# Kernel optimization log

Hardware: AMD Instinct MI355X
Metric: run time of the kernel (lower is better)

Reference implementation:

```python
import jax, jax.numpy as jnp
import numpy as np

S, B, E, H = 512, 64, 256, 256


def _cell(h, c, xt, wih, whh, bih, bhh):
    # PyTorch LSTM gate order: i, f, g, o
    z = xt @ wih.T + h @ whh.T + bih + bhh  # (B, 4H)
    i, f, g, o = jnp.split(z, 4, axis=-1)
    c = jax.nn.sigmoid(f) * c + jax.nn.sigmoid(i) * jnp.tanh(g)
    h = jax.nn.sigmoid(o) * jnp.tanh(c)
    return h, c


def _bilstm(x, h0, c0, wih_f, whh_f, bih_f, bhh_f, wih_b, whh_b, bih_b, bhh_b):
    # x: (T,B,E); h0,c0: (2,B,H) -> out (T,B,2H), hn/cn (2,B,H)
    def fstep(carry, xt):
        h, c = _cell(carry[0], carry[1], xt, wih_f, whh_f, bih_f, bhh_f)
        return (h, c), h

    def bstep(carry, xt):
        h, c = _cell(carry[0], carry[1], xt, wih_b, whh_b, bih_b, bhh_b)
        return (h, c), h

    (hf, cf), out_f = jax.lax.scan(fstep, (h0[0], c0[0]), x)
    (hb, cb), out_b_rev = jax.lax.scan(bstep, (h0[1], c0[1]), x[::-1])
    out = jnp.concatenate([out_f, out_b_rev[::-1]], axis=-1)
    return out, jnp.stack([hf, hb]), jnp.stack([cf, cb])


def setup_inputs() -> dict:
    key = jax.random.key(0)
    ks = jax.random.split(key, 9)
    s = 1.0 / np.sqrt(H)
    u = lambda k, shape: jax.random.uniform(k, shape, jnp.float32, -s, s)
    return {
        "inputs": jax.random.normal(ks[0], (S, B, E), jnp.float32),
        "wih_f": u(ks[1], (4 * H, E)), "whh_f": u(ks[2], (4 * H, H)),
        "bih_f": u(ks[3], (4 * H,)), "bhh_f": u(ks[4], (4 * H,)),
        "wih_b": u(ks[5], (4 * H, E)), "whh_b": u(ks[6], (4 * H, H)),
        "bih_b": u(ks[7], (4 * H,)), "bhh_b": u(ks[8], (4 * H,)),
    }


def reference(inputs, wih_f, whh_f, bih_f, bhh_f, wih_b, whh_b, bih_b, bhh_b):
    seq, batch = inputs.shape[0], inputs.shape[1]
    params = (wih_f, whh_f, bih_f, bhh_f, wih_b, whh_b, bih_b, bhh_b)
    # windows i=0..S-2 are each 2 tokens: inputs[i:i+2]
    windows = jnp.stack([inputs[:-1], inputs[1:]], axis=1)  # (S-1, 2, B, E)

    def step(carry, win):
        h, c = carry
        out, hn, cn = _bilstm(win, h, c, *params)
        return (hn, cn), out  # out (2,B,2H)

    h0 = jnp.zeros((2, batch, H), inputs.dtype)
    c0 = jnp.zeros((2, batch, H), inputs.dtype)
    (hl, cl), outs = jax.lax.scan(step, (h0, c0), windows)
    # final window i=S-1 is length 1, seeded with the state from window S-2
    out_last, _, _ = _bilstm(inputs[-1:], hl, cl, *params)  # (1,B,2H)
    hidden = jnp.concatenate(
        [outs.reshape(2 * (seq - 1), batch, 2 * H), out_last], axis=0
    )  # (2S-1, B, 2H)
    # AdaptiveMaxPool1d(1) over the time axis
    emb = hidden.max(axis=0)  # (B, 2H)
    return emb
```

## Files before the change

kernel.cpp:

```cpp
#include <hip/hip_runtime.h>

typedef __attribute__((ext_vector_type(8))) short short8;
typedef __attribute__((ext_vector_type(4))) float f32x4;
typedef __attribute__((ext_vector_type(4))) unsigned short u16x4;
typedef __attribute__((ext_vector_type(4))) unsigned int u32x4;

#define S_ 512
#define B_ 64
#define E_ 256
#define H_ 256
#define NSTEP 1023

__device__ __forceinline__ unsigned short f2bf(float f) {
  unsigned u = __builtin_bit_cast(unsigned, f);
  return (unsigned short)((u + 0x7fffu + ((u >> 16) & 1u)) >> 16);
}
__device__ __forceinline__ float bf2f(unsigned short h) {
  unsigned u = ((unsigned)h) << 16;
  return __builtin_bit_cast(float, u);
}
__device__ __forceinline__ float sigm(float x) { return 1.f / (1.f + __expf(-x)); }
__device__ __forceinline__ float tanh_(float x) {
  x = fminf(fmaxf(x, -15.f), 15.f);
  float e = __expf(-2.f * x);
  return (1.f - e) / (1.f + e);
}

__global__ __launch_bounds__(256) void prep9(
    const float* __restrict__ x,
    const float* __restrict__ wih_f, const float* __restrict__ whh_f,
    const float* __restrict__ bih_f, const float* __restrict__ bhh_f,
    const float* __restrict__ wih_b, const float* __restrict__ whh_b,
    const float* __restrict__ bih_b, const float* __restrict__ bhh_b,
    short* __restrict__ x_bf, short* __restrict__ wx, short* __restrict__ wh,
    float* __restrict__ bias_p)
{
  long i0 = (long)blockIdx.x * blockDim.x + threadIdx.x;
  long stride = (long)gridDim.x * blockDim.x;
  const long NX = (long)S_ * B_ * E_;
  const long NW = 2L * 1024 * 256;
  const long NB = 2L * 1024;

  for (long i = i0; i < NX; i += stride) x_bf[i] = (short)f2bf(x[i]);

  for (long i = i0; i < NW; i += stride) {
    int ch  = (int)(i >> 18);
    int rem = (int)(i & 262143);
    int p   = rem >> 8;
    int k   = rem & 255;
    int jc  = p >> 2, g = p & 3;
    long j  = (long)(g * 256 + jc);
    wx[i] = (short)f2bf((ch ? wih_b : wih_f)[j * 256 + k]);
    wh[i] = (short)f2bf((ch ? whh_b : whh_f)[j * 256 + k]);
  }

  for (long i = i0; i < NB; i += stride) {
    int ch = (int)(i >> 10);
    int p  = (int)(i & 1023);
    int jc = p >> 2, g = p & 3;
    int j  = g * 256 + jc;
    bias_p[i] = ch ? (bih_b[j] + bhh_b[j]) : (bih_f[j] + bhh_f[j]);
  }
}

__global__ __launch_bounds__(512, 2) void xz_gemm9(
    const short* __restrict__ x_bf, const short* __restrict__ wx,
    const float* __restrict__ bias_p, short* __restrict__ xz)
{
  const int bid = blockIdx.x;
  const int ch = bid >> 9, t = bid & 511;
  const int tid = threadIdx.x;
  const int wave = tid >> 6, lane = tid & 63;
  const int l15 = lane & 15, l4 = lane >> 4;

  const short* W = wx + (long)ch * 1024 * 256;
  const short* X = x_bf + (long)t * B_ * E_;

  f32x4 acc[8][4];
#pragma unroll
  for (int mt = 0; mt < 8; ++mt)
#pragma unroll
    for (int nt = 0; nt < 4; ++nt) acc[mt][nt] = (f32x4){0.f, 0.f, 0.f, 0.f};

#pragma unroll
  for (int ks = 0; ks < 8; ++ks) {
    int k0 = ks * 32 + l4 * 8;
    short8 bfr[4];
#pragma unroll
    for (int nt = 0; nt < 4; ++nt)
      bfr[nt] = *(const short8*)(X + (long)(nt * 16 + l15) * E_ + k0);
#pragma unroll
    for (int mt = 0; mt < 8; ++mt) {
      int p = (wave * 8 + mt) * 16 + l15;
      short8 af = *(const short8*)(W + (long)p * 256 + k0);
#pragma unroll
      for (int nt = 0; nt < 4; ++nt)
        acc[mt][nt] = __builtin_amdgcn_mfma_f32_16x16x32_bf16(af, bfr[nt], acc[mt][nt], 0, 0, 0);
    }
  }

#pragma unroll
  for (int mt = 0; mt < 8; ++mt) {
    int jc = (wave * 8 + mt) * 4 + l4;
    f32x4 b4 = *(const f32x4*)(bias_p + ch * 1024 + jc * 4);
#pragma unroll
    for (int nt = 0; nt < 4; ++nt) {
      int b = nt * 16 + l15;
      u16x4 v;
#pragma unroll
      for (int g = 0; g < 4; ++g) v[g] = f2bf(acc[mt][nt][g] + b4[g]);
      long off = (((long)(ch * 512 + t) * 256 + jc) * 64 + b) * 4;
      *(u16x4*)(xz + off) = v;
    }
  }
}

__global__ __launch_bounds__(512) void lstm10(
    const short* __restrict__ wh, const short* __restrict__ xz,
    short* __restrict__ hring, float* __restrict__ out)
{
  const int bid  = blockIdx.x;
  const int ch   = bid >> 4;
  const int bs   = (bid >> 2) & 3;
  const int role = bid & 3;
  const int tid  = threadIdx.x;
  const int wave = tid >> 6, lane = tid & 63;
  const int l15 = lane & 15, l4 = lane >> 4;

  __shared__ short hin[16 * 256];
  __shared__ short hout[16 * 64];

  const short* whc = wh + (long)ch * 1024 * 256;

  short8 ah[2][8];
#pragma unroll
  for (int mt = 0; mt < 2; ++mt)
#pragma unroll
    for (int ks = 0; ks < 8; ++ks)
      ah[mt][ks] = *(const short8*)(whc + (long)(role * 256 + wave * 32 + mt * 16 + l15) * 256 + ks * 32 + l4 * 8);

  float cst[2], hmax[2];
#pragma unroll
  for (int mt = 0; mt < 2; ++mt) { cst[mt] = 0.f; hmax[mt] = -2.f; }

  short* rb = hring + ch * 16384;
  const int swzr = (l15 & 7) << 4;

  const int sb = tid >> 4, sc = tid & 15;
  const int pb = tid >> 5, pc = tid & 31;

  for (int t = 0; t < NSTEP; ++t) {
    int tok;
    if (ch == 0) tok = (t + 1) >> 1;
    else         tok = (t == NSTEP - 1) ? (S_ - 1) : ((t & 1) ? (t >> 1) : (t >> 1) + 1);

    u16x4 xq[2];
#pragma unroll
    for (int mt = 0; mt < 2; ++mt) {
      int jc = role * 64 + wave * 8 + mt * 4 + l4;
      long off = (((long)(ch * 512 + tok) * 256 + jc) * 64 + (bs * 16 + l15)) * 4;
      xq[mt] = *(const u16x4*)(xz + off);
    }

    if (tid < 256) {
      short* pa = rb + ((t + 1) & 3) * 32768 + (bs * 16 + sb) * 256 + role * 64 + sc * 4;
      unsigned long long pv = 0xFFFFFFFFFFFFFFFFull;
      asm volatile("global_store_dwordx2 %0, %1, off sc1" :: "v"(pa), "v"(pv) : "memory");
    }

    {
      const short* ga = rb + ((t + 3) & 3) * 32768 + (bs * 16 + pb) * 256 + pc * 8;
      short8 hv;
      int ok;
      do {
        asm volatile("global_load_dwordx4 %0, %1, off sc1\n\ts_waitcnt vmcnt(0)"
                     : "=v"(hv) : "v"(ga) : "memory");
        u32x4 dv = __builtin_bit_cast(u32x4, hv);
        ok = (dv.x != 0xFFFFFFFFu) & (dv.y != 0xFFFFFFFFu) &
             (dv.z != 0xFFFFFFFFu) & (dv.w != 0xFFFFFFFFu);
      } while (__ballot(!ok));
      *(short8*)((char*)hin + pb * 512 + ((pc * 16) ^ ((pb & 7) << 4))) = hv;
    }
    __syncthreads();

    f32x4 acc[2];
    acc[0] = (f32x4){0.f, 0.f, 0.f, 0.f};
    acc[1] = (f32x4){0.f, 0.f, 0.f, 0.f};
    const char* hr = (const char*)hin + l15 * 512;
#pragma unroll
    for (int ks = 0; ks < 8; ++ks) {
      short8 hfr = *(const short8*)(hr + ((ks * 64 + l4 * 16) ^ swzr));
      acc[0] = __builtin_amdgcn_mfma_f32_16x16x32_bf16(ah[0][ks], hfr, acc[0], 0, 0, 0);
      acc[1] = __builtin_amdgcn_mfma_f32_16x16x32_bf16(ah[1][ks], hfr, acc[1], 0, 0, 0);
    }

#pragma unroll
    for (int mt = 0; mt < 2; ++mt) {
      float zi = acc[mt][0] + bf2f(xq[mt][0]);
      float zf = acc[mt][1] + bf2f(xq[mt][1]);
      float zg = acc[mt][2] + bf2f(xq[mt][2]);
      float zo = acc[mt][3] + bf2f(xq[mt][3]);
      float cc = cst[mt];
      cc = sigm(zf) * cc + sigm(zi) * tanh_(zg);
      float hh = sigm(zo) * tanh_(cc);
      cst[mt] = cc;
      hmax[mt] = fmaxf(hmax[mt], hh);
      int lc = wave * 8 + mt * 4 + l4;
      *(short*)((char*)hout + l15 * 128 + ((lc * 2) ^ ((l15 & 7) << 4))) = (short)f2bf(hh);
    }
    __syncthreads();

    if (tid < 256) {
      unsigned long long val =
          *(const unsigned long long*)((const char*)hout + sb * 128 + ((sc * 8) ^ ((sb & 7) << 4)));
      short* ga = rb + (t & 3) * 32768 + (bs * 16 + sb) * 256 + role * 64 + sc * 4;
      asm volatile("global_store_dwordx2 %0, %1, off sc1" :: "v"(ga), "v"(val) : "memory");
    }
  }

#pragma unroll
  for (int mt = 0; mt < 2; ++mt) {
    int jc = role * 64 + wave * 8 + mt * 4 + l4;
    out[(long)(bs * 16 + l15) * (2 * H_) + ch * H_ + jc] = hmax[mt];
  }
}

extern "C" void kernel_launch(void* const* d_in, const int* in_sizes, int n_in,
                              void* d_out, int out_size, void* d_ws, size_t ws_size,
                              hipStream_t stream) {
  const float* x     = (const float*)d_in[0];
  const float* wih_f = (const float*)d_in[1];
  const float* whh_f = (const float*)d_in[2];
  const float* bih_f = (const float*)d_in[3];
  const float* bhh_f = (const float*)d_in[4];
  const float* wih_b = (const float*)d_in[5];
  const float* whh_b = (const float*)d_in[6];
  const float* bih_b = (const float*)d_in[7];
  const float* bhh_b = (const float*)d_in[8];

  char* ws = (char*)d_ws;
  short* x_bf   = (short*)(ws);
  short* hring  = (short*)(ws);
  short* wx     = (short*)(ws + 16777216);
  short* wh     = (short*)(ws + 17825792);
  float* bias_p = (float*)(ws + 18874368);
  short* xz     = (short*)(ws + 18882560);

  const size_t NEED = 18882560UL + 134217728UL;
  if (ws_size < NEED) return;

  prep9<<<2048, 256, 0, stream>>>(x, wih_f, whh_f, bih_f, bhh_f,
                                  wih_b, whh_b, bih_b, bhh_b,
                                  x_bf, wx, wh, bias_p);
  xz_gemm9<<<1024, 512, 0, stream>>>(x_bf, wx, bias_p, xz);

  hipMemsetAsync(ws, 0xFF, 196608, stream);
  hipMemsetAsync(ws + 196608, 0, 65536, stream);

  lstm10<<<32, 512, 0, stream>>>(wh, xz, hring, (float*)d_out);
}
```

Baseline: 1.824 ms.

## Write own hidden slice to double-buffered LDS and drop second barrier

Each block now writes its own newly computed hidden slice straight into a double-buffered LDS tile and stores it to the global ring with per-lane 16-bit stores. This removes the staging buffer and the second __syncthreads per step. Polling loads skip the block's own columns, and the sentinel check now works per 16-bit element. The trade is many small scattered global stores in place of coalesced 8-byte stores, which may add memory traffic on the critical recurrent path.

```diff
diff --git a/kernel.cpp b/kernel.cpp
--- a/kernel.cpp
+++ b/kernel.cpp
@@ -115,7 +115,7 @@
   }
 }
 
-__global__ __launch_bounds__(512) void lstm10(
+__global__ __launch_bounds__(512) void lstm12(
     const short* __restrict__ wh, const short* __restrict__ xz,
     short* __restrict__ hring, float* __restrict__ out)
 {
@@ -127,8 +127,9 @@
   const int wave = tid >> 6, lane = tid & 63;
   const int l15 = lane & 15, l4 = lane >> 4;
 
-  __shared__ short hin[16 * 256];
-  __shared__ short hout[16 * 64];
+  __shared__ short hin[2][16 * 256];
+
+  for (int i = tid; i < 2 * 16 * 256; i += 512) ((short*)hin)[i] = 0;
 
   const short* whc = wh + (long)ch * 1024 * 256;
 
@@ -148,6 +149,9 @@
 
   const int sb = tid >> 4, sc = tid & 15;
   const int pb = tid >> 5, pc = tid & 31;
+  const int own = (pc >> 3) == role;
+
+  __syncthreads();
 
   for (int t = 0; t < NSTEP; ++t) {
     int tok;
@@ -171,22 +175,29 @@
     {
       const short* ga = rb + ((t + 3) & 3) * 32768 + (bs * 16 + pb) * 256 + pc * 8;
       short8 hv;
-      int ok;
+      int bad;
       do {
-        asm volatile("global_load_dwordx4 %0, %1, off sc1\n\ts_waitcnt vmcnt(0)"
-                     : "=v"(hv) : "v"(ga) : "memory");
-        u32x4 dv = __builtin_bit_cast(u32x4, hv);
-        ok = (dv.x != 0xFFFFFFFFu) & (dv.y != 0xFFFFFFFFu) &
-             (dv.z != 0xFFFFFFFFu) & (dv.w != 0xFFFFFFFFu);
-      } while (__ballot(!ok));
-      *(short8*)((char*)hin + pb * 512 + ((pc * 16) ^ ((pb & 7) << 4))) = hv;
+        bad = 0;
+        if (!own) {
+          asm volatile("global_load_dwordx4 %0, %1, off sc1\n\ts_waitcnt vmcnt(0)"
+                       : "=v"(hv) : "v"(ga) : "memory");
+          u32x4 dv = __builtin_bit_cast(u32x4, hv);
+#pragma unroll
+          for (int i = 0; i < 4; ++i) {
+            unsigned d = dv[i];
+            bad |= ((d & 0xFFFFu) == 0xFFFFu) | ((d >> 16) == 0xFFFFu);
+          }
+        }
+      } while (__ballot(bad));
+      if (!own)
+        *(short8*)((char*)hin[t & 1] + pb * 512 + ((pc * 16) ^ ((pb & 7) << 4))) = hv;
     }
     __syncthreads();
 
     f32x4 acc[2];
     acc[0] = (f32x4){0.f, 0.f, 0.f, 0.f};
     acc[1] = (f32x4){0.f, 0.f, 0.f, 0.f};
-    const char* hr = (const char*)hin + l15 * 512;
+    const char* hr = (const char*)hin[t & 1] + l15 * 512;
 #pragma unroll
     for (int ks = 0; ks < 8; ++ks) {
       short8 hfr = *(const short8*)(hr + ((ks * 64 + l4 * 16) ^ swzr));
@@ -194,6 +205,8 @@
       acc[1] = __builtin_amdgcn_mfma_f32_16x16x32_bf16(ah[1][ks], hfr, acc[1], 0, 0, 0);
     }
 
+    short* rslot = rb + (t & 3) * 32768 + (bs * 16 + l15) * 256;
+    char* hnext = (char*)hin[(t + 1) & 1] + l15 * 512;
 #pragma unroll
     for (int mt = 0; mt < 2; ++mt) {
       float zi = acc[mt][0] + bf2f(xq[mt][0]);
@@ -205,16 +218,12 @@
       float hh = sigm(zo) * tanh_(cc);
       cst[mt] = cc;
       hmax[mt] = fmaxf(hmax[mt], hh);
-      int lc = wave * 8 + mt * 4 + l4;
-      *(short*)((char*)hout + l15 * 128 + ((lc * 2) ^ ((l15 & 7) << 4))) = (short)f2bf(hh);
-    }
-    __syncthreads();
-
-    if (tid < 256) {
-      unsigned long long val =
-          *(const unsigned long long*)((const char*)hout + sb * 128 + ((sc * 8) ^ ((sb & 7) << 4)));
-      short* ga = rb + (t & 3) * 32768 + (bs * 16 + sb) * 256 + role * 64 + sc * 4;
-      asm volatile("global_store_dwordx2 %0, %1, off sc1" :: "v"(ga), "v"(val) : "memory");
+      unsigned short hb = f2bf(hh);
+      int col = role * 64 + wave * 8 + mt * 4 + l4;
+      *(short*)(hnext + ((col * 2) ^ swzr)) = (short)hb;
+      unsigned hv32 = (unsigned)hb;
+      short* ga = rslot + col;
+      asm volatile("global_store_short %0, %1, off sc1" :: "v"(ga), "v"(hv32) : "memory");
     }
   }
 
@@ -257,5 +266,5 @@
   hipMemsetAsync(ws, 0xFF, 196608, stream);
   hipMemsetAsync(ws + 196608, 0, 65536, stream);
 
-  lstm10<<<32, 512, 0, stream>>>(wh, xz, hring, (float*)d_out);
-}
+  lstm12<<<32, 512, 0, stream>>>(wh, xz, hring, (float*)d_out);
+}
```

New measurement: 2.099 ms. +15.1%, slower.
